# Optimization experiments

Measured on AMD Instinct MI355X. Metric: run time of the kernel, lower is better.

The kernel has to match this reference:

```python
import jax, jax.numpy as jnp
import numpy as np

L, B = 512, 32
N_IN, D, N_OUT, NL = 72, 512, 144, 5  # D = n_hidden per direction


def setup_inputs() -> dict:
    key = jax.random.key(0)
    ks = jax.random.split(key, 16)
    def rn(k, shape, scale=1.0):
        return jax.random.normal(k, shape, dtype=jnp.float32) * scale
    return {
        "x": rn(ks[0], (L, B, N_IN)),
        "lin1_w": rn(ks[1], (N_IN, D), N_IN ** -0.5),
        "lin1_b": rn(ks[2], (D,), 0.1),
        "lin2_w": rn(ks[3], (2 * D, N_OUT), (2 * D) ** -0.5),
        "lin2_b": rn(ks[4], (N_OUT,), 0.1),
        "W0": rn(ks[5], (D, 2 * D * 4), D ** -0.5),          # layer 0: k=4
        "wc0": rn(ks[6], (2, 2, D), 0.5),                    # (fgt/rst, dir, D)
        "b0": rn(ks[7], (2, 2, D), 0.1),
        "ln0_g": 1.0 + rn(ks[8], (D,), 0.1),
        "ln0_b": rn(ks[9], (D,), 0.1),
        "Wl": rn(ks[10], (NL - 1, 2 * D, 2 * D * 3), (2 * D) ** -0.5),  # k=3
        "wcl": rn(ks[11], (NL - 1, 2, 2, D), 0.5),
        "bl": rn(ks[12], (NL - 1, 2, 2, D), 0.1),
        "lnl_g": 1.0 + rn(ks[13], (NL - 1, 2 * D), 0.1),
        "lnl_b": rn(ks[14], (NL - 1, 2 * D), 0.1),
    }


def _layer_norm(x, g, b):
    m = x.mean(-1, keepdims=True)
    v = x.var(-1, keepdims=True)
    return (x - m) * jax.lax.rsqrt(v + 1e-5) * g + b


def _sru_layer(x, W, wc, b, k):
    """Bidirectional SRU cell. x: (L,B,in); W: (in, 2*D*k); wc,b: (2,2,D).
    U layout (sru lib): (L, B, dir, D, k) with slices [cand, forget, reset(, residual)].
    f_t = sig(U1 + v_f*c_{t-1} + b_f); c_t = f*c_{t-1} + (1-f)*U0;
    r_t = sig(U2 + v_r*c_t + b_r); h_t = r*c_t + (1-r)*res  (identity activation).
    """
    Lx, Bx = x.shape[0], x.shape[1]
    U = (x @ W).reshape(Lx, Bx, 2, D, k)
    Uf, Ub = U[:, :, 0], U[:, :, 1][::-1]  # backward dir: flip time
    if k == 4:
        resf, resb = Uf[..., 3], Ub[..., 3]
    else:  # k==3: residual is the input itself, split per direction
        resf, resb = x[..., :D], x[..., D:][::-1]
    pack = lambda a, c: jnp.stack([a, c], axis=1)  # (L,2,B,D)
    u0 = pack(Uf[..., 0], Ub[..., 0])
    u1 = pack(Uf[..., 1], Ub[..., 1])
    u2 = pack(Uf[..., 2], Ub[..., 2])
    res = pack(resf, resb)
    wcf, wcr = wc[0][:, None, :], wc[1][:, None, :]  # (2,1,D) broadcast over B
    bf, br = b[0][:, None, :], b[1][:, None, :]
    c0 = jnp.zeros((2, Bx, D), x.dtype)

    def step(c, t):
        tu0, tu1, tu2, tres = t
        f = jax.nn.sigmoid(tu1 + wcf * c + bf)
        c = f * c + (1.0 - f) * tu0
        r = jax.nn.sigmoid(tu2 + wcr * c + br)
        h = r * c + (1.0 - r) * tres
        return c, h

    c_fin, hs = jax.lax.scan(step, c0, (u0, u1, u2, res))  # hs: (L,2,B,D)
    out = jnp.concatenate([hs[:, 0], hs[:, 1][::-1]], axis=-1)  # (L,B,2D)
    c_cat = jnp.concatenate([c_fin[0], c_fin[1]], axis=-1)      # (B,2D)
    return out, c_cat


def reference(x, lin1_w, lin1_b, lin2_w, lin2_b, W0, wc0, b0, ln0_g, ln0_b,
              Wl, wcl, bl, lnl_g, lnl_b):
    # dropout layers are identity in eval mode
    y = jax.nn.relu(x @ lin1_w + lin1_b)
    cs = []
    y, c = _sru_layer(_layer_norm(y, ln0_g, ln0_b), W0, wc0, b0, 4)
    cs.append(c)
    for i in range(NL - 1):
        y, c = _sru_layer(_layer_norm(y, lnl_g[i], lnl_b[i]), Wl[i], wcl[i], bl[i], 3)
        cs.append(c)
    out = y @ lin2_w + lin2_b  # (L,B,N_OUT)
    return out, jnp.stack(cs)  # h: (NL, B, 2D)
```

## Files before the change

kernel.cpp:

```cpp
#include <hip/hip_runtime.h>
#include <hip/hip_bf16.h>
#include <hip/hip_fp16.h>

typedef _Float16 f16;
typedef f16 f16x8 __attribute__((ext_vector_type(8)));
typedef float f32x4 __attribute__((ext_vector_type(4)));

#define LL 512
#define BB 32
#define DD 512
#define MM (LL * BB)

__device__ __forceinline__ void gl16(const f16* g, f16* l) {
  __builtin_amdgcn_global_load_lds(
      (const __attribute__((address_space(1))) void*)g,
      (__attribute__((address_space(3))) void*)l, 16, 0, 0);
}

template <int KS>
__global__ __launch_bounds__(256) void k_transpose_perm(const float* __restrict__ in,
                                                        f16* __restrict__ out, int K, int N) {
  __shared__ float tile[32][33];
  size_t bo = (size_t)blockIdx.z * (size_t)K * N;
  const int PD = 512 * KS;
  int n0 = blockIdx.x * 32, k0 = blockIdx.y * 32;
  int tx = threadIdx.x, ty = threadIdx.y;
#pragma unroll
  for (int s = 0; s < 4; ++s)
    tile[ty + s * 8][tx] = in[bo + (size_t)(k0 + ty + s * 8) * N + n0 + tx];
  __syncthreads();
#pragma unroll
  for (int s = 0; s < 4; ++s) {
    int n = n0 + ty + s * 8;
    int dir = n / PD, w = n % PD;
    int orow = dir * PD + (w % KS) * 512 + (w / KS);
    out[bo + (size_t)orow * K + k0 + tx] = (f16)tile[tx][ty + s * 8];
  }
}

__global__ __launch_bounds__(256) void k_transpose2(const float* __restrict__ in,
                                                    f16* __restrict__ out) {
  __shared__ float tile[32][33];
  int n0 = blockIdx.x * 32, k0 = blockIdx.y * 32;
  int tx = threadIdx.x, ty = threadIdx.y;
#pragma unroll
  for (int s = 0; s < 4; ++s) {
    int n = n0 + tx;
    tile[ty + s * 8][tx] = (n < 144) ? in[(size_t)(k0 + ty + s * 8) * 144 + n] : 0.f;
  }
  __syncthreads();
#pragma unroll
  for (int s = 0; s < 4; ++s) {
    int n = n0 + ty + s * 8;
    if (n < 144) out[(size_t)n * 1024 + k0 + tx] = (f16)tile[tx][ty + s * 8];
  }
}

__global__ __launch_bounds__(256) void k_lin1(const float* __restrict__ x,
                                              const float* __restrict__ w,
                                              const float* __restrict__ bias,
                                              f16* __restrict__ yH) {
  __shared__ float xs[8][72];
  int m0 = blockIdx.x * 8;
  int t = threadIdx.x;
  if (t < 144) {
    int row = t / 18, c4 = (t % 18) * 4;
    float4 v = *(const float4*)(x + (size_t)(m0 + row) * 72 + c4);
    xs[row][c4] = v.x; xs[row][c4 + 1] = v.y; xs[row][c4 + 2] = v.z; xs[row][c4 + 3] = v.w;
  }
  __syncthreads();
  int j0 = t, j1 = t + 256;
  float b0 = bias[j0], b1 = bias[j1];
  float acc[8][2];
#pragma unroll
  for (int r = 0; r < 8; ++r) { acc[r][0] = b0; acc[r][1] = b1; }
  for (int k = 0; k < 72; ++k) {
    float w0 = w[k * 512 + j0], w1 = w[k * 512 + j1];
#pragma unroll
    for (int r = 0; r < 8; ++r) {
      acc[r][0] = fmaf(xs[r][k], w0, acc[r][0]);
      acc[r][1] = fmaf(xs[r][k], w1, acc[r][1]);
    }
  }
#pragma unroll
  for (int r = 0; r < 8; ++r) {
    yH[(size_t)(m0 + r) * 512 + j0] = (f16)fmaxf(acc[r][0], 0.f);
    yH[(size_t)(m0 + r) * 512 + j1] = (f16)fmaxf(acc[r][1], 0.f);
  }
}

template <int W>
__global__ __launch_bounds__(256) void k_ln(const f16* __restrict__ in,
                                            const float* __restrict__ g,
                                            const float* __restrict__ be,
                                            f16* __restrict__ out) {
  constexpr int V = W / 256;
  int row = blockIdx.x, t = threadIdx.x;
  const f16* p = in + (size_t)row * W + t * V;
  float v[V];
  if constexpr (V == 4) {
    union { uint2 u; f16 h[4]; } pk;
    pk.u = *(const uint2*)p;
#pragma unroll
    for (int i = 0; i < 4; ++i) v[i] = (float)pk.h[i];
  } else {
    union { unsigned u; f16 h[2]; } pk;
    pk.u = *(const unsigned*)p;
    v[0] = (float)pk.h[0]; v[1] = (float)pk.h[1];
  }
  float s = 0.f, ss = 0.f;
#pragma unroll
  for (int i = 0; i < V; ++i) { s += v[i]; ss += v[i] * v[i]; }
#pragma unroll
  for (int o = 32; o > 0; o >>= 1) { s += __shfl_down(s, o); ss += __shfl_down(ss, o); }
  __shared__ float red[10];
  if ((t & 63) == 0) { red[(t >> 6) * 2] = s; red[(t >> 6) * 2 + 1] = ss; }
  __syncthreads();
  if (t == 0) {
    float S = red[0] + red[2] + red[4] + red[6];
    float SS = red[1] + red[3] + red[5] + red[7];
    float mean = S / W;
    float var = SS / W - mean * mean;
    red[8] = mean; red[9] = rsqrtf(var + 1e-5f);
  }
  __syncthreads();
  float mean = red[8], rstd = red[9];
  if constexpr (V == 4) {
    union { f16 h[4]; uint2 u; } pk;
#pragma unroll
    for (int i = 0; i < 4; ++i) {
      int col = t * 4 + i;
      pk.h[i] = (f16)((v[i] - mean) * rstd * g[col] + be[col]);
    }
    *(uint2*)(out + (size_t)row * W + t * 4) = pk.u;
  } else {
    union { f16 h[2]; unsigned u; } pk;
#pragma unroll
    for (int i = 0; i < 2; ++i) {
      int col = t * 2 + i;
      pk.h[i] = (f16)((v[i] - mean) * rstd * g[col] + be[col]);
    }
    *(unsigned*)(out + (size_t)row * W + t * 2) = pk.u;
  }
}

template <int K>
__global__ __launch_bounds__(256, 2) void k_gemm(const f16* __restrict__ A,
                                                 const f16* __restrict__ BT,
                                                 f16* __restrict__ C, int N) {
  __shared__ __align__(16) f16 lA[128 * 32];
  __shared__ __align__(16) f16 lB[128 * 32];
  int n0 = blockIdx.x * 128, m0 = blockIdx.y * 128;
  int tid = threadIdx.x, lane = tid & 63, wave = tid >> 6;
  int wr = wave >> 1, wc = wave & 1;
  int fr = lane & 15, kq = (lane >> 4) * 8;
  f32x4 acc[4][4] = {};

  int srow = wave * 32 + (lane >> 2);
  int skel = (lane & 3) * 8;
  const f16* Ap0 = A + (size_t)(m0 + srow) * K + skel;
  const f16* Ap1 = Ap0 + (size_t)16 * K;
  const f16* Bp0 = BT + (size_t)(n0 + srow) * K + skel;
  const f16* Bp1 = Bp0 + (size_t)16 * K;
  f16* lA0 = lA + wave * 1024; f16* lA1 = lA0 + 512;
  f16* lB0 = lB + wave * 1024; f16* lB1 = lB0 + 512;

  for (int k0 = 0; k0 < K; k0 += 32) {
    if (k0) __syncthreads();
    gl16(Ap0 + k0, lA0); gl16(Ap1 + k0, lA1);
    gl16(Bp0 + k0, lB0); gl16(Bp1 + k0, lB1);
    __syncthreads();
    f16x8 af[4], bf[4];
#pragma unroll
    for (int i = 0; i < 4; ++i) af[i] = *(const f16x8*)&lA[(wr * 64 + i * 16 + fr) * 32 + kq];
#pragma unroll
    for (int j = 0; j < 4; ++j) bf[j] = *(const f16x8*)&lB[(wc * 64 + j * 16 + fr) * 32 + kq];
#pragma unroll
    for (int i = 0; i < 4; ++i)
#pragma unroll
      for (int j = 0; j < 4; ++j)
        acc[i][j] = __builtin_amdgcn_mfma_f32_16x16x32_f16(af[i], bf[j], acc[i][j], 0, 0, 0);
  }
  int col = n0 + wc * 64 + fr;
  int rb = m0 + wr * 64 + (lane >> 4) * 4;
#pragma unroll
  for (int i = 0; i < 4; ++i)
#pragma unroll
    for (int j = 0; j < 4; ++j)
#pragma unroll
      for (int r = 0; r < 4; ++r)
        C[(size_t)(rb + i * 16 + r) * N + col + j * 16] = (f16)acc[i][j][r];
}

template <int KK>
__global__ __launch_bounds__(64) void k_scan(const f16* __restrict__ U,
                                             const f16* __restrict__ xln,
                                             const float* __restrict__ wcp,
                                             const float* __restrict__ bp,
                                             f16* __restrict__ yH,
                                             float* __restrict__ cs) {
  int tid = blockIdx.x * 64 + threadIdx.x;
  int dir = tid >> 14, b = (tid >> 9) & 31, d = tid & 511;
  int col = (dir << 9) + d;
  const int N = 1024 * KK;
  const f16* base = U + dir * (512 * KK) + d;
  const f16* rbase = (KK == 4) ? base + 1536 : xln + col;
  const long rstride = (KK == 4) ? N : 1024;
  float wcf = wcp[col], wcr = wcp[1024 + col];
  float bfv = bp[col], brv = bp[1024 + col];
  float c = 0.f;
  f16 ru0[8], ru1[8], ru2[8], rr[8];
  float hh[16];

  const long sgn = dir ? -32L : 32L;
  const long sN = sgn * N, sR = sgn * rstride, sY = sgn * 1024;
  long row0 = ((long)(dir ? 511 : 0) << 5) + b;
  const f16* pL = base + (size_t)row0 * N;
  const f16* pR = rbase + (size_t)row0 * rstride;
#pragma unroll
  for (int i = 0; i < 8; ++i) {
    ru0[i] = pL[0]; ru1[i] = pL[512]; ru2[i] = pL[1024];
    rr[i] = *pR;
    pL += sN; pR += sR;
  }
  f16* pS = yH + (size_t)row0 * 1024 + col;

#define BODY(i, DO_STORE, DO_PRE)                                        \
  {                                                                      \
    float u0 = (float)ru0[(i) & 7], u1 = (float)ru1[(i) & 7],            \
          u2 = (float)ru2[(i) & 7], res = (float)rr[(i) & 7];            \
    if (DO_STORE) {                                                      \
      *pS = (f16)hh[((i) + 8) & 15];                                     \
      pS += sY;                                                          \
      __builtin_amdgcn_sched_barrier(0);  \
    }                                                                    \
    if (DO_PRE) {                                                        \
      ru0[(i) & 7] = pL[0]; ru1[(i) & 7] = pL[512];                      \
      ru2[(i) & 7] = pL[1024]; rr[(i) & 7] = *pR;                        \
      pL += sN; pR += sR;                                                \
    }                                                                    \
    float zf = u1 + wcf * c + bfv;                                       \
    float f = __builtin_amdgcn_rcpf(1.f + __expf(-zf));                  \
    c = f * c + (1.f - f) * u0;                                          \
    float zr = u2 + wcr * c + brv;                                       \
    float r = __builtin_amdgcn_rcpf(1.f + __expf(-zr));                  \
    hh[(i) & 15] = r * c + (1.f - r) * res;                              \
  }

#pragma unroll
  for (int i = 0; i < 16; ++i) BODY(i, (i >= 8), true);
  for (int t0 = 16; t0 < 496; t0 += 16) {
#pragma unroll
    for (int i = 0; i < 16; ++i) BODY(i, true, true);
  }
#pragma unroll
  for (int i = 0; i < 16; ++i) BODY(i, true, (i < 8));
#pragma unroll
  for (int j = 8; j < 16; ++j) { *pS = (f16)hh[j]; pS += sY; }
  cs[b * 1024 + col] = c;
#undef BODY
}

__global__ __launch_bounds__(256) void k_lin2m(const f16* __restrict__ Y,
                                               const f16* __restrict__ WT,
                                               const float* __restrict__ bias,
                                               float* __restrict__ out) {
  __shared__ __align__(16) f16 lA[64 * 32];
  int m0 = blockIdx.x * 64;
  int tid = threadIdx.x, lane = tid & 63, wave = tid >> 6;
  int fr = lane & 15, kq = (lane >> 4) * 8;
  f32x4 acc[9] = {};
  int srow = wave * 16 + (lane >> 2);
  int skel = (lane & 3) * 8;
  const f16* Yp = Y + (size_t)(m0 + srow) * 1024 + skel;
  f16* ldst = lA + wave * 512;
  for (int k0 = 0; k0 < 1024; k0 += 32) {
    if (k0) __syncthreads();
    gl16(Yp + k0, ldst);
    f16x8 bf[9];
#pragma unroll
    for (int j = 0; j < 9; ++j)
      bf[j] = *(const f16x8*)(WT + (size_t)(j * 16 + fr) * 1024 + k0 + kq);
    __syncthreads();
    f16x8 af = *(const f16x8*)&lA[(wave * 16 + fr) * 32 + kq];
#pragma unroll
    for (int j = 0; j < 9; ++j)
      acc[j] = __builtin_amdgcn_mfma_f32_16x16x32_f16(af, bf[j], acc[j], 0, 0, 0);
  }
  int rb = m0 + wave * 16 + (lane >> 4) * 4;
#pragma unroll
  for (int j = 0; j < 9; ++j) {
    float bv = bias[j * 16 + fr];
#pragma unroll
    for (int r = 0; r < 4; ++r)
      out[(size_t)(rb + r) * 144 + j * 16 + fr] = acc[j][r] + bv;
  }
}

extern "C" void kernel_launch(void* const* d_in, const int* in_sizes, int n_in,
                              void* d_out, int out_size, void* d_ws, size_t ws_size,
                              hipStream_t stream) {
  const float* x      = (const float*)d_in[0];
  const float* lin1_w = (const float*)d_in[1];
  const float* lin1_b = (const float*)d_in[2];
  const float* lin2_w = (const float*)d_in[3];
  const float* lin2_b = (const float*)d_in[4];
  const float* W0     = (const float*)d_in[5];
  const float* wc0    = (const float*)d_in[6];
  const float* b0     = (const float*)d_in[7];
  const float* ln0_g  = (const float*)d_in[8];
  const float* ln0_b  = (const float*)d_in[9];
  const float* Wl     = (const float*)d_in[10];
  const float* wcl    = (const float*)d_in[11];
  const float* bl     = (const float*)d_in[12];
  const float* lnl_g  = (const float*)d_in[13];
  const float* lnl_b  = (const float*)d_in[14];
  float* out = (float*)d_out;

  char* ws = (char*)d_ws;
  f16* yH  = (f16*)(ws);
  f16* A16 = (f16*)(ws + ((size_t)32 << 20));
  f16* C16 = (f16*)(ws + ((size_t)64 << 20));
  f16* WT2 = (f16*)(ws + ((size_t)192 << 20));
  f16* W0T = (f16*)(ws + ((size_t)224 << 20));
  f16* WlT = (f16*)(ws + ((size_t)228 << 20));

  k_transpose_perm<4><<<dim3(128, 16, 1), dim3(32, 8), 0, stream>>>(W0, W0T, 512, 4096);
  k_transpose_perm<3><<<dim3(96, 32, 4), dim3(32, 8), 0, stream>>>(Wl, WlT, 1024, 3072);

  k_lin1<<<MM / 8, 256, 0, stream>>>(x, lin1_w, lin1_b, yH);

  k_ln<512><<<MM, 256, 0, stream>>>(yH, ln0_g, ln0_b, A16);
  k_gemm<512><<<dim3(32, 128), 256, 0, stream>>>(A16, W0T, C16, 4096);
  k_scan<4><<<512, 64, 0, stream>>>(C16, (const f16*)nullptr, wc0, b0, yH, out + 2359296);

  k_transpose2<<<dim3(5, 32), dim3(32, 8), 0, stream>>>(lin2_w, WT2);

  for (int i = 0; i < 4; ++i) {
    k_ln<1024><<<MM, 256, 0, stream>>>(yH, lnl_g + i * 1024, lnl_b + i * 1024, A16);
    k_gemm<1024><<<dim3(24, 128), 256, 0, stream>>>(A16, WlT + (size_t)i * 3072 * 1024, C16, 3072);
    k_scan<3><<<512, 64, 0, stream>>>(C16, A16, wcl + i * 2048, bl + i * 2048, yH,
                                      out + 2359296 + (size_t)(i + 1) * 32768);
  }

  k_lin2m<<<MM / 64, 256, 0, stream>>>(yH, WT2, lin2_b, out);
}
```

Before: 1.125 ms.

## Pipeline GEMM with 4-stage LDS ring, fragment layout and XCD-aware block remap

Replaces the single-buffered GEMM with a 4-slot LDS ring that prefetches three K-tiles ahead using async global-to-LDS loads and fine-grained vmcnt waits, so only one barrier is needed per iteration. The LDS layout is rearranged so each lane's MFMA fragment is a contiguous 16-byte read, which avoids bank conflicts. Workgroup IDs are remapped across the 8 XCDs for cache locality, and wave priority is raised around the MFMA block. This raises LDS use to 64KB per block, which may limit occupancy.

```diff
diff --git a/kernel.cpp b/kernel.cpp
--- a/kernel.cpp
+++ b/kernel.cpp
@@ -145,44 +145,80 @@
 }
 
 template <int K>
-__global__ __launch_bounds__(256, 2) void k_gemm(const f16* __restrict__ A,
-                                                 const f16* __restrict__ BT,
-                                                 f16* __restrict__ C, int N) {
-  __shared__ __align__(16) f16 lA[128 * 32];
-  __shared__ __align__(16) f16 lB[128 * 32];
-  int n0 = blockIdx.x * 128, m0 = blockIdx.y * 128;
-  int tid = threadIdx.x, lane = tid & 63, wave = tid >> 6;
-  int wr = wave >> 1, wc = wave & 1;
-  int fr = lane & 15, kq = (lane >> 4) * 8;
+__global__ __launch_bounds__(256, 2) void k_gemmp(const f16* __restrict__ A,
+                                                  const f16* __restrict__ BT,
+                                                  f16* __restrict__ C, int N) {
+  constexpr int NT = K / 32;
+  __shared__ __align__(16) f16 lds[32768];
+  const int tid = threadIdx.x, lane = tid & 63, wave = tid >> 6;
+  const int wr = wave >> 1, wc = wave & 1;
+
+  const int nx = gridDim.x;
+  int nwg = nx * gridDim.y;
+  int bid = blockIdx.y * nx + blockIdx.x;
+  int wg = (bid & 7) * (nwg >> 3) + (bid >> 3);
+  int n0 = (wg % nx) * 128, m0 = (wg / nx) * 128;
+
+  const int r1 = ((tid >> 6) << 4) | (tid & 15);
+  const int c1 = (tid >> 4) & 3;
+  const f16* Asrc = A + (size_t)(m0 + r1) * K + c1 * 8;
+  const f16* Bsrc = BT + (size_t)(n0 + r1) * K + c1 * 8;
+  const int K64 = 64 * K;
+
+  const int rdA = ((lane >> 4) << 4) | (lane & 15);
+  const int fA = wr * 2048 + rdA * 8;
+  const int fB = 16384 + wc * 2048 + rdA * 8;
+
   f32x4 acc[4][4] = {};
 
-  int srow = wave * 32 + (lane >> 2);
-  int skel = (lane & 3) * 8;
-  const f16* Ap0 = A + (size_t)(m0 + srow) * K + skel;
-  const f16* Ap1 = Ap0 + (size_t)16 * K;
-  const f16* Bp0 = BT + (size_t)(n0 + srow) * K + skel;
-  const f16* Bp1 = Bp0 + (size_t)16 * K;
-  f16* lA0 = lA + wave * 1024; f16* lA1 = lA0 + 512;
-  f16* lB0 = lB + wave * 1024; f16* lB1 = lB0 + 512;
-
-  for (int k0 = 0; k0 < K; k0 += 32) {
-    if (k0) __syncthreads();
-    gl16(Ap0 + k0, lA0); gl16(Ap1 + k0, lA1);
-    gl16(Bp0 + k0, lB0); gl16(Bp1 + k0, lB1);
-    __syncthreads();
-    f16x8 af[4], bf[4];
-#pragma unroll
-    for (int i = 0; i < 4; ++i) af[i] = *(const f16x8*)&lA[(wr * 64 + i * 16 + fr) * 32 + kq];
-#pragma unroll
-    for (int j = 0; j < 4; ++j) bf[j] = *(const f16x8*)&lB[(wc * 64 + j * 16 + fr) * 32 + kq];
-#pragma unroll
-    for (int i = 0; i < 4; ++i)
-#pragma unroll
-      for (int j = 0; j < 4; ++j)
-        acc[i][j] = __builtin_amdgcn_mfma_f32_16x16x32_f16(af[i], bf[j], acc[i][j], 0, 0, 0);
-  }
+#define STAGE(t)                                                \
+  {                                                             \
+    const f16* a_ = Asrc + (t) * 32;                            \
+    const f16* b_ = Bsrc + (t) * 32;                            \
+    f16* d_ = lds + (((t) & 3) << 12) + wave * 512;             \
+    gl16(a_, d_);                                               \
+    gl16(a_ + K64, d_ + 2048);                                  \
+    gl16(b_, d_ + 16384);                                       \
+    gl16(b_ + K64, d_ + 18432);                                 \
+  }
+
+  STAGE(0) STAGE(1) STAGE(2)
+  asm volatile("s_waitcnt vmcnt(8)" ::: "memory");
+  __builtin_amdgcn_s_barrier();
+
+#define GITER(t, DOSTAGE, VMN, DOBAR)                                         \
+  {                                                                           \
+    if (DOSTAGE) STAGE((t) + 3);                                              \
+    const int sb = (((t) & 3) << 12);                                         \
+    f16x8 af[4], bf[4];                                                       \
+    _Pragma("unroll") for (int i = 0; i < 4; ++i)                             \
+        af[i] = *(const f16x8*)&lds[sb + fA + i * 512];                       \
+    _Pragma("unroll") for (int j = 0; j < 4; ++j)                             \
+        bf[j] = *(const f16x8*)&lds[sb + fB + j * 512];                       \
+    __builtin_amdgcn_s_setprio(1);                                            \
+    _Pragma("unroll") for (int i = 0; i < 4; ++i)                             \
+        _Pragma("unroll") for (int j = 0; j < 4; ++j)                         \
+            acc[i][j] = __builtin_amdgcn_mfma_f32_16x16x32_f16(               \
+                af[i], bf[j], acc[i][j], 0, 0, 0);                            \
+    __builtin_amdgcn_s_setprio(0);                                            \
+    __builtin_amdgcn_sched_barrier(0);                                        \
+    if ((VMN) == 8) { asm volatile("s_waitcnt vmcnt(8)" ::: "memory"); }      \
+    else if ((VMN) == 4) { asm volatile("s_waitcnt vmcnt(4)" ::: "memory"); } \
+    else if ((VMN) == 0) { asm volatile("s_waitcnt vmcnt(0)" ::: "memory"); } \
+    if (DOBAR) __builtin_amdgcn_s_barrier();                                  \
+  }
+
+#pragma unroll 1
+  for (int t = 0; t < NT - 3; ++t) GITER(t, true, 8, true)
+  GITER(NT - 3, false, 4, true)
+  GITER(NT - 2, false, 0, true)
+  GITER(NT - 1, false, -1, false)
+#undef GITER
+#undef STAGE
+
+  const int fr = lane & 15, q = lane >> 4;
   int col = n0 + wc * 64 + fr;
-  int rb = m0 + wr * 64 + (lane >> 4) * 4;
+  int rb = m0 + wr * 64 + q * 4;
 #pragma unroll
   for (int i = 0; i < 4; ++i)
 #pragma unroll
@@ -232,7 +268,7 @@
     if (DO_STORE) {                                                      \
       *pS = (f16)hh[((i) + 8) & 15];                                     \
       pS += sY;                                                          \
-      __builtin_amdgcn_sched_barrier(0);  \
+      __builtin_amdgcn_sched_barrier(0);                                 \
     }                                                                    \
     if (DO_PRE) {                                                        \
       ru0[(i) & 7] = pL[0]; ru1[(i) & 7] = pL[512];                      \
@@ -331,14 +367,14 @@
   k_lin1<<<MM / 8, 256, 0, stream>>>(x, lin1_w, lin1_b, yH);
 
   k_ln<512><<<MM, 256, 0, stream>>>(yH, ln0_g, ln0_b, A16);
-  k_gemm<512><<<dim3(32, 128), 256, 0, stream>>>(A16, W0T, C16, 4096);
+  k_gemmp<512><<<dim3(32, 128), 256, 0, stream>>>(A16, W0T, C16, 4096);
   k_scan<4><<<512, 64, 0, stream>>>(C16, (const f16*)nullptr, wc0, b0, yH, out + 2359296);
 
   k_transpose2<<<dim3(5, 32), dim3(32, 8), 0, stream>>>(lin2_w, WT2);
 
   for (int i = 0; i < 4; ++i) {
     k_ln<1024><<<MM, 256, 0, stream>>>(yH, lnl_g + i * 1024, lnl_b + i * 1024, A16);
-    k_gemm<1024><<<dim3(24, 128), 256, 0, stream>>>(A16, WlT + (size_t)i * 3072 * 1024, C16, 3072);
+    k_gemmp<1024><<<dim3(24, 128), 256, 0, stream>>>(A16, WlT + (size_t)i * 3072 * 1024, C16, 3072);
     k_scan<3><<<512, 64, 0, stream>>>(C16, A16, wcl + i * 2048, bl + i * 2048, yH,
                                       out + 2359296 + (size_t)(i + 1) * 32768);
   }
```

Result: slower. 1.424 ms (+26.6%).
